# Kernel optimization log

Hardware: AMD Instinct MI355X
Metric: run time of the kernel (lower is better)

The kernel has to match this reference:

```python
import jax, jax.numpy as jnp
import numpy as np

N = 50000
IN_C = 128
HID = 64
HEADS = 4
OUT_C = 64
E_RAND = 800000
NEG_SLOPE = 0.2  # PyG GATConv default


def setup_inputs() -> dict:
    key = jax.random.key(0)
    ks = jax.random.split(key, 10)
    x = jax.random.normal(ks[0], (N, IN_C), dtype=jnp.float32)
    src = jax.random.randint(ks[1], (E_RAND,), 0, N)
    dst = jax.random.randint(ks[2], (E_RAND,), 0, N)
    loops = jnp.arange(N)
    # PyG GATConv adds self-loops by default; append them here
    edge_index = jnp.stack([jnp.concatenate([src, loops]),
                            jnp.concatenate([dst, loops])], axis=0).astype(jnp.int64)
    s = 0.05
    W1 = jax.random.normal(ks[3], (IN_C, HEADS * HID), dtype=jnp.float32) * s
    att_src1 = jax.random.normal(ks[4], (HEADS, HID), dtype=jnp.float32) * s
    att_dst1 = jax.random.normal(ks[5], (HEADS, HID), dtype=jnp.float32) * s
    b1 = jnp.zeros((HEADS * HID,), dtype=jnp.float32)
    W2 = jax.random.normal(ks[6], (HEADS * HID, OUT_C), dtype=jnp.float32) * s
    att_src2 = jax.random.normal(ks[7], (1, OUT_C), dtype=jnp.float32) * s
    att_dst2 = jax.random.normal(ks[8], (1, OUT_C), dtype=jnp.float32) * s
    b2 = jnp.zeros((OUT_C,), dtype=jnp.float32)
    return {"x": x, "edge_index": edge_index, "W1": W1, "att_src1": att_src1,
            "att_dst1": att_dst1, "b1": b1, "W2": W2, "att_src2": att_src2,
            "att_dst2": att_dst2, "b2": b2}


def gat_conv(x, src, dst, W, att_src, att_dst, bias, heads, ch, concat):
    n = x.shape[0]
    h = (x @ W).reshape(n, heads, ch)                      # [N,H,C]
    a_src = jnp.einsum('nhc,hc->nh', h, att_src)           # [N,H]
    a_dst = jnp.einsum('nhc,hc->nh', h, att_dst)
    e = jax.nn.leaky_relu(a_src[src] + a_dst[dst], NEG_SLOPE)  # [E,H]
    # segment softmax over incoming edges of each dst node
    m = jax.ops.segment_max(e, dst, num_segments=n)
    ex = jnp.exp(e - m[dst])
    ssum = jax.ops.segment_sum(ex, dst, num_segments=n)
    alpha = ex / jnp.where(ssum[dst] > 0, ssum[dst], 1.0)  # [E,H]
    msg = h[src] * alpha[:, :, None]                        # [E,H,C]
    out = jax.ops.segment_sum(msg, dst, num_segments=n)     # [N,H,C]
    out = out.reshape(n, heads * ch) if concat else out.mean(axis=1)
    return out + bias


def reference(x, edge_index, W1, att_src1, att_dst1, b1, W2, att_src2, att_dst2, b2):
    src, dst = edge_index[0], edge_index[1]
    # eval mode: feature dropout and attention dropout are identity
    h = gat_conv(x, src, dst, W1, att_src1, att_dst1, b1, HEADS, HID, True)
    h = jax.nn.elu(h)
    out = gat_conv(h, src, dst, W2, att_src2, att_dst2, b2, 1, OUT_C, False)
    return out
```

## Files before the change

kernel.cpp:

```cpp
#include <hip/hip_runtime.h>
#include <hip/hip_bf16.h>

#define IN_C 128
#define HID 64
#define HEADS 4
#define OUT_C 64
#define NEG_SLOPE 0.2f

typedef __attribute__((ext_vector_type(8))) short bfrag8;
typedef __attribute__((ext_vector_type(4))) float facc4;

__device__ __forceinline__ float bf16u_to_f(unsigned short u) {
  return __uint_as_float(((unsigned)u) << 16);
}
__device__ __forceinline__ unsigned short f_to_bf16u(float f) {
  return __bfloat16_as_ushort(__float2bfloat16(f));
}
__device__ __forceinline__ float leaky(float x) {
  return (x > 0.f) ? x : NEG_SLOPE * x;
}

__global__ __launch_bounds__(256) void cvt_w_kernel(
    const float* __restrict__ W1, const float* __restrict__ W2,
    unsigned short* __restrict__ B1img, unsigned short* __restrict__ B2img) {
  int i = blockIdx.x * 256 + threadIdx.x;
  if (i < 4096) {
    int g = i & 7, n = (i >> 3) & 255, kt = i >> 11;
    unsigned short q[8];
#pragma unroll
    for (int e = 0; e < 8; ++e)
      q[e] = f_to_bf16u(W1[(size_t)(kt * 64 + g * 8 + e) * 256 + n]);
    *reinterpret_cast<uint4*>(&B1img[kt * 16384 + n * 64 + ((g ^ (n & 7)) << 3)]) =
        *reinterpret_cast<const uint4*>(q);
  } else if (i < 4096 + 2048) {
    int j = i - 4096;
    int g = j & 7, n = (j >> 3) & 63, kt = j >> 9;
    unsigned short q[8];
#pragma unroll
    for (int e = 0; e < 8; ++e)
      q[e] = f_to_bf16u(W2[(size_t)(kt * 64 + g * 8 + e) * 64 + n]);
    *reinterpret_cast<uint4*>(&B2img[kt * 4096 + n * 64 + ((g ^ (n & 7)) << 3)]) =
        *reinterpret_cast<const uint4*>(q);
  }
}

__global__ __launch_bounds__(256) void mfma_gemm1_wide(
    const float* __restrict__ A, const unsigned short* __restrict__ B1img,
    const float* __restrict__ att_src, const float* __restrict__ att_dst,
    unsigned short* __restrict__ Hout, float* __restrict__ a_src,
    float* __restrict__ a_dst, int M) {
  __shared__ unsigned short As[64 * 64];
  __shared__ unsigned short Bs[256 * 64];
  const int t = threadIdx.x;
  const int wid = t >> 6, lane = t & 63;
  const int lg = lane >> 4, li = lane & 15;
  const int bm = blockIdx.x * 64;

  facc4 acc[16];
#pragma unroll
  for (int fn = 0; fn < 16; ++fn) acc[fn] = (facc4)(0.f);

#pragma unroll
  for (int kt = 0; kt < 2; ++kt) {
#pragma unroll
    for (int p = 0; p < 2; ++p) {
      int flat = t + p * 256;
      int row = flat >> 3, g = flat & 7;
      int gr = bm + row;
      float4 v0 = make_float4(0.f, 0.f, 0.f, 0.f), v1 = v0;
      if (gr < M) {
        const float* src = &A[(size_t)gr * 128 + kt * 64 + g * 8];
        v0 = *reinterpret_cast<const float4*>(src);
        v1 = *reinterpret_cast<const float4*>(src + 4);
      }
      unsigned short q[8];
      q[0] = f_to_bf16u(v0.x); q[1] = f_to_bf16u(v0.y);
      q[2] = f_to_bf16u(v0.z); q[3] = f_to_bf16u(v0.w);
      q[4] = f_to_bf16u(v1.x); q[5] = f_to_bf16u(v1.y);
      q[6] = f_to_bf16u(v1.z); q[7] = f_to_bf16u(v1.w);
      *reinterpret_cast<uint4*>(&As[row * 64 + ((g ^ (row & 7)) << 3)]) =
          *reinterpret_cast<const uint4*>(q);
    }
#pragma unroll
    for (int p = 0; p < 8; ++p) {
      int gi = t + p * 256;
      *reinterpret_cast<uint4*>(&Bs[gi * 8]) =
          *reinterpret_cast<const uint4*>(&B1img[kt * 16384 + gi * 8]);
    }
    __syncthreads();
#pragma unroll
    for (int ks = 0; ks < 2; ++ks) {
      int arow = wid * 16 + li;
      int gk = ks * 4 + lg;
      bfrag8 a = *reinterpret_cast<const bfrag8*>(
          &As[arow * 64 + ((gk ^ (arow & 7)) << 3)]);
#pragma unroll
      for (int fn = 0; fn < 16; ++fn) {
        int col = fn * 16 + li;
        bfrag8 b = *reinterpret_cast<const bfrag8*>(
            &Bs[col * 64 + ((gk ^ (col & 7)) << 3)]);
        acc[fn] =
            __builtin_amdgcn_mfma_f32_16x16x32_bf16(a, b, acc[fn], 0, 0, 0);
      }
    }
    __syncthreads();
  }

#pragma unroll
  for (int reg = 0; reg < 4; ++reg) {
    int row = bm + wid * 16 + lg * 4 + reg;
    if (row < M) {
#pragma unroll
      for (int fn = 0; fn < 16; ++fn)
        Hout[(size_t)row * 256 + fn * 16 + li] = f_to_bf16u(acc[fn][reg]);
    }
#pragma unroll
    for (int h = 0; h < 4; ++h) {
      float ps = 0.f, pd = 0.f;
#pragma unroll
      for (int q = 0; q < 4; ++q) {
        int fn = h * 4 + q;
        float c = acc[fn][reg];
        ps += c * att_src[fn * 16 + li];
        pd += c * att_dst[fn * 16 + li];
      }
#pragma unroll
      for (int m = 1; m < 16; m <<= 1) {
        ps += __shfl_xor(ps, m);
        pd += __shfl_xor(pd, m);
      }
      if (row < M && li == 0) {
        a_src[(size_t)row * 4 + h] = ps;
        a_dst[(size_t)row * 4 + h] = pd;
      }
    }
  }
}

__global__ __launch_bounds__(256) void mfma_gemm2(
    const unsigned short* __restrict__ A, const unsigned short* __restrict__ B2img,
    const float* __restrict__ att_src, const float* __restrict__ att_dst,
    unsigned short* __restrict__ Hout, float* __restrict__ a_src,
    float* __restrict__ a_dst, int M) {
  __shared__ unsigned short As[64 * 64];
  __shared__ unsigned short Bs[64 * 64];
  const int t = threadIdx.x;
  const int wid = t >> 6, lane = t & 63;
  const int lg = lane >> 4, li = lane & 15;
  const int bm = blockIdx.x * 64;

  facc4 acc[4];
#pragma unroll
  for (int fn = 0; fn < 4; ++fn) acc[fn] = (facc4)(0.f);

#pragma unroll
  for (int kt = 0; kt < 4; ++kt) {
#pragma unroll
    for (int p = 0; p < 2; ++p) {
      int flat = t + p * 256;
      int row = flat >> 3, g = flat & 7;
      int gr = bm + row;
      uint4 v = make_uint4(0, 0, 0, 0);
      if (gr < M)
        v = *reinterpret_cast<const uint4*>(&A[(size_t)gr * 256 + kt * 64 + g * 8]);
      *reinterpret_cast<uint4*>(&As[row * 64 + ((g ^ (row & 7)) << 3)]) = v;
    }
#pragma unroll
    for (int p = 0; p < 2; ++p) {
      int gi = t + p * 256;
      *reinterpret_cast<uint4*>(&Bs[gi * 8]) =
          *reinterpret_cast<const uint4*>(&B2img[kt * 4096 + gi * 8]);
    }
    __syncthreads();
#pragma unroll
    for (int ks = 0; ks < 2; ++ks) {
      int arow = wid * 16 + li;
      int gk = ks * 4 + lg;
      bfrag8 a = *reinterpret_cast<const bfrag8*>(
          &As[arow * 64 + ((gk ^ (arow & 7)) << 3)]);
#pragma unroll
      for (int fn = 0; fn < 4; ++fn) {
        int col = fn * 16 + li;
        bfrag8 b = *reinterpret_cast<const bfrag8*>(
            &Bs[col * 64 + ((gk ^ (col & 7)) << 3)]);
        acc[fn] =
            __builtin_amdgcn_mfma_f32_16x16x32_bf16(a, b, acc[fn], 0, 0, 0);
      }
    }
    __syncthreads();
  }

  float s_att[4], d_att[4];
#pragma unroll
  for (int fn = 0; fn < 4; ++fn) {
    s_att[fn] = att_src[fn * 16 + li];
    d_att[fn] = att_dst[fn * 16 + li];
  }
#pragma unroll
  for (int reg = 0; reg < 4; ++reg) {
    int row = bm + wid * 16 + lg * 4 + reg;
    float ps = 0.f, pd = 0.f;
#pragma unroll
    for (int fn = 0; fn < 4; ++fn) {
      float c = acc[fn][reg];
      ps += c * s_att[fn];
      pd += c * d_att[fn];
    }
#pragma unroll
    for (int m = 1; m < 16; m <<= 1) {
      ps += __shfl_xor(ps, m);
      pd += __shfl_xor(pd, m);
    }
    if (row < M) {
#pragma unroll
      for (int fn = 0; fn < 4; ++fn)
        Hout[(size_t)row * 64 + fn * 16 + li] = f_to_bf16u(acc[fn][reg]);
      if (li == 0) {
        a_src[row] = ps;
        a_dst[row] = pd;
      }
    }
  }
}

__global__ void hist_kernel(const int* __restrict__ dst, int E,
                            int* __restrict__ deg) {
  int e = blockIdx.x * blockDim.x + threadIdx.x;
  if (e < E) atomicAdd(&deg[dst[e]], 1);
}

__device__ __forceinline__ int pad4(int d) { return (d + 3) & ~3; }

__global__ __launch_bounds__(256) void scan_partial_kernel(
    const int* __restrict__ deg, int n, int* __restrict__ partials) {
  __shared__ int sm[256];
  int t = threadIdx.x;
  int i = blockIdx.x * 256 + t;
  sm[t] = (i < n) ? pad4(deg[i]) : 0;
  __syncthreads();
  for (int off = 128; off > 0; off >>= 1) {
    if (t < off) sm[t] += sm[t + off];
    __syncthreads();
  }
  if (t == 0) partials[blockIdx.x] = sm[0];
}

__global__ __launch_bounds__(256) void scan_expand_kernel(
    const int* __restrict__ deg, int n, const int* __restrict__ partials,
    int nb, int* __restrict__ offsets, int* __restrict__ cursor,
    int* __restrict__ ssrc) {
  __shared__ int smp[256];
  __shared__ int sm[256];
  int t = threadIdx.x;
  smp[t] = (t < nb) ? partials[t] : 0;
  __syncthreads();
  for (int off = 1; off < 256; off <<= 1) {
    int u = (t >= off) ? smp[t - off] : 0;
    __syncthreads();
    smp[t] += u;
    __syncthreads();
  }
  int base = (blockIdx.x > 0) ? smp[blockIdx.x - 1] : 0;
  int i = blockIdx.x * 256 + t;
  int d = (i < n) ? deg[i] : 0;
  int v = pad4(d);
  sm[t] = v;
  __syncthreads();
  for (int off = 1; off < 256; off <<= 1) {
    int u = (t >= off) ? sm[t - off] : 0;
    __syncthreads();
    sm[t] += u;
    __syncthreads();
  }
  int excl = sm[t] - v + base;
  if (i < n) {
    offsets[i] = excl;
    cursor[i] = excl;
    for (int k = d; k < v; ++k) ssrc[excl + k] = -1;
  }
}

__global__ void scatter_kernel(const int* __restrict__ src,
                               const int* __restrict__ dst, int E,
                               int* __restrict__ cursor,
                               int* __restrict__ ssrc) {
  int e = blockIdx.x * blockDim.x + threadIdx.x;
  if (e < E) {
    int d = dst[e];
    int pos = atomicAdd(&cursor[d], 1);
    ssrc[pos] = src[e];
  }
}

__global__ __launch_bounds__(256) void agg1_kernel(
    const unsigned short* __restrict__ h1, const float* __restrict__ as1,
    const float* __restrict__ ad1, const int* __restrict__ ssrc,
    const int* __restrict__ offsets, const int* __restrict__ deg,
    const float* __restrict__ bias, unsigned short* __restrict__ out,
    int n_nodes) {
  int wave = (int)((blockIdx.x * blockDim.x + threadIdx.x) >> 6);
  int lane = threadIdx.x & 63;
  if (wave >= n_nodes) return;
  int head = lane >> 4;
  int off = offsets[wave];
  int cnt = deg[wave];
  int last = ((cnt + 3) >> 2) - 1;
  const int* S_ = ssrc + off;
  float ad = ad1[wave * 4 + head];
  const int pbase = lane & 48;

  auto ldS = [&](int g) {
    return *reinterpret_cast<const int4*>(S_ + min(g, last) * 4);
  };
  auto gK = [&](int4 S, float* a_out) {
    int sk = (lane & 1) ? S.y : S.x;
    int sk2 = (lane & 1) ? S.w : S.z;
    sk = (lane & 2) ? sk2 : sk;
    *a_out = as1[max(sk, 0) * 4 + head];
    return sk;
  };
  auto mkP = [&](int sk, float a) {
    float pk = (sk >= 0) ? __expf(leaky(a + ad)) : 0.f;
    return make_float4(__shfl(pk, pbase), __shfl(pk, pbase + 1),
                       __shfl(pk, pbase + 2), __shfl(pk, pbase + 3));
  };
  auto gat = [&](int s) {
    return *reinterpret_cast<const ushort4*>(
        &h1[(size_t)max(s, 0) * 256 + lane * 4]);
  };

  int4 Sg0 = ldS(0), Sg1 = ldS(1), Sg2 = ldS(2), Sg3 = ldS(3);
  ushort4 H0 = gat(Sg0.x), H1 = gat(Sg0.y), H2 = gat(Sg0.z), H3 = gat(Sg0.w);
  ushort4 H4 = gat(Sg1.x), H5 = gat(Sg1.y), H6 = gat(Sg1.z), H7 = gat(Sg1.w);
  ushort4 H8 = gat(Sg2.x), H9 = gat(Sg2.y), H10 = gat(Sg2.z), H11 = gat(Sg2.w);
  float aK0, aK1, aK2;
  int sk0 = gK(Sg0, &aK0);
  int sk1 = gK(Sg1, &aK1);
  int sk2 = gK(Sg2, &aK2);
  float4 P0 = mkP(sk0, aK0), P1v = mkP(sk1, aK1);

  float l = 0.f, a0 = 0.f, a1 = 0.f, a2 = 0.f, a3 = 0.f;
  for (int j = 0; j <= last; ++j) {
    int4 Sg4 = ldS(j + 4);
    float aK3;
    int sk3 = gK(Sg3, &aK3);
    float4 P2v = mkP(sk2, aK2);
    l += P0.x + P0.y + P0.z + P0.w;
    a0 += P0.x * bf16u_to_f(H0.x) + P0.y * bf16u_to_f(H1.x) +
          P0.z * bf16u_to_f(H2.x) + P0.w * bf16u_to_f(H3.x);
    a1 += P0.x * bf16u_to_f(H0.y) + P0.y * bf16u_to_f(H1.y) +
          P0.z * bf16u_to_f(H2.y) + P0.w * bf16u_to_f(H3.y);
    a2 += P0.x * bf16u_to_f(H0.z) + P0.y * bf16u_to_f(H1.z) +
          P0.z * bf16u_to_f(H2.z) + P0.w * bf16u_to_f(H3.z);
    a3 += P0.x * bf16u_to_f(H0.w) + P0.y * bf16u_to_f(H1.w) +
          P0.z * bf16u_to_f(H2.w) + P0.w * bf16u_to_f(H3.w);
    H0 = H4; H1 = H5; H2 = H6; H3 = H7;
    H4 = H8; H5 = H9; H6 = H10; H7 = H11;
    H8 = gat(Sg3.x); H9 = gat(Sg3.y); H10 = gat(Sg3.z); H11 = gat(Sg3.w);
    Sg3 = Sg4;
    sk2 = sk3; aK2 = aK3;
    P0 = P1v; P1v = P2v;
  }
  float inv = 1.0f / l;
  int col = lane * 4;
  float4 b4 = *reinterpret_cast<const float4*>(&bias[col]);
  float o0 = a0 * inv + b4.x;
  float o1 = a1 * inv + b4.y;
  float o2 = a2 * inv + b4.z;
  float o3 = a3 * inv + b4.w;
  o0 = o0 > 0.f ? o0 : __expf(o0) - 1.f;
  o1 = o1 > 0.f ? o1 : __expf(o1) - 1.f;
  o2 = o2 > 0.f ? o2 : __expf(o2) - 1.f;
  o3 = o3 > 0.f ? o3 : __expf(o3) - 1.f;
  unsigned short q[4];
  q[0] = f_to_bf16u(o0); q[1] = f_to_bf16u(o1);
  q[2] = f_to_bf16u(o2); q[3] = f_to_bf16u(o3);
  *reinterpret_cast<ushort4*>(&out[(size_t)wave * 256 + col]) =
      *reinterpret_cast<const ushort4*>(q);
}

__global__ __launch_bounds__(256) void agg2_kernel(
    const unsigned short* __restrict__ h2, const float* __restrict__ as2,
    const float* __restrict__ ad2, const int* __restrict__ ssrc,
    const int* __restrict__ offsets, const int* __restrict__ deg,
    const float* __restrict__ bias, float* __restrict__ out, int n_nodes) {
  int wave = (int)((blockIdx.x * blockDim.x + threadIdx.x) >> 6);
  int lane = threadIdx.x & 63;
  if (wave >= n_nodes) return;
  int off = offsets[wave];
  int cnt = deg[wave];
  int last = ((cnt + 3) >> 2) - 1;
  const int* S_ = ssrc + off;
  float ad = ad2[wave];

  auto ldS = [&](int g) {
    return *reinterpret_cast<const int4*>(S_ + min(g, last) * 4);
  };
  auto gK = [&](int4 S, float* a_out) {
    int sk = (lane & 1) ? S.y : S.x;
    int sk2 = (lane & 1) ? S.w : S.z;
    sk = (lane & 2) ? sk2 : sk;
    *a_out = as2[max(sk, 0)];
    return sk;
  };
  auto mkP = [&](int sk, float a) {
    float pk = (sk >= 0) ? __expf(leaky(a + ad)) : 0.f;
    return make_float4(__shfl(pk, 0), __shfl(pk, 1), __shfl(pk, 2),
                       __shfl(pk, 3));
  };
  auto gat = [&](int s) { return h2[(size_t)max(s, 0) * 64 + lane]; };

  int4 Sg0 = ldS(0), Sg1 = ldS(1), Sg2 = ldS(2), Sg3 = ldS(3);
  unsigned short H0 = gat(Sg0.x), H1 = gat(Sg0.y), H2 = gat(Sg0.z),
                 H3 = gat(Sg0.w);
  unsigned short H4 = gat(Sg1.x), H5 = gat(Sg1.y), H6 = gat(Sg1.z),
                 H7 = gat(Sg1.w);
  unsigned short H8 = gat(Sg2.x), H9 = gat(Sg2.y), H10 = gat(Sg2.z),
                 H11 = gat(Sg2.w);
  float aK0, aK1, aK2;
  int sk0 = gK(Sg0, &aK0);
  int sk1 = gK(Sg1, &aK1);
  int sk2 = gK(Sg2, &aK2);
  float4 P0 = mkP(sk0, aK0), P1v = mkP(sk1, aK1);

  float l = 0.f, acc = 0.f;
  for (int j = 0; j <= last; ++j) {
    int4 Sg4 = ldS(j + 4);
    float aK3;
    int sk3 = gK(Sg3, &aK3);
    float4 P2v = mkP(sk2, aK2);
    l += P0.x + P0.y + P0.z + P0.w;
    acc += P0.x * bf16u_to_f(H0) + P0.y * bf16u_to_f(H1) +
           P0.z * bf16u_to_f(H2) + P0.w * bf16u_to_f(H3);
    H0 = H4; H1 = H5; H2 = H6; H3 = H7;
    H4 = H8; H5 = H9; H6 = H10; H7 = H11;
    H8 = gat(Sg3.x); H9 = gat(Sg3.y); H10 = gat(Sg3.z); H11 = gat(Sg3.w);
    Sg3 = Sg4;
    sk2 = sk3; aK2 = aK3;
    P0 = P1v; P1v = P2v;
  }
  out[(size_t)wave * 64 + lane] = acc / l + bias[lane];
}

extern "C" void kernel_launch(void* const* d_in, const int* in_sizes, int n_in,
                              void* d_out, int out_size, void* d_ws,
                              size_t ws_size, hipStream_t stream) {
  const float* x = (const float*)d_in[0];
  const int* edge_index = (const int*)d_in[1];
  const float* W1 = (const float*)d_in[2];
  const float* att_src1 = (const float*)d_in[3];
  const float* att_dst1 = (const float*)d_in[4];
  const float* b1 = (const float*)d_in[5];
  const float* W2 = (const float*)d_in[6];
  const float* att_src2 = (const float*)d_in[7];
  const float* att_dst2 = (const float*)d_in[8];
  const float* b2 = (const float*)d_in[9];

  const int n = in_sizes[0] / IN_C;
  const int E = in_sizes[1] / 2;
  const int* src = edge_index;
  const int* dst = edge_index + E;
  const int nb = (n + 255) / 256;
  const int stride = (E + 4 * n + 3) & ~3;

  char* ws = (char*)d_ws;
  size_t off = 0;
  auto carve = [&](size_t bytes) -> void* {
    void* p = ws + off;
    off = (off + bytes + 255) & ~(size_t)255;
    return p;
  };
  unsigned short* h1b = (unsigned short*)carve((size_t)n * 256 * 2);
  unsigned short* hact = (unsigned short*)carve((size_t)n * 256 * 2);
  unsigned short* h2b = (unsigned short*)carve((size_t)n * 64 * 2);
  unsigned short* B1img = (unsigned short*)carve(32768 * 2);
  unsigned short* B2img = (unsigned short*)carve(16384 * 2);
  float* as1 = (float*)carve((size_t)n * 4 * 4);
  float* ad1 = (float*)carve((size_t)n * 4 * 4);
  float* as2 = (float*)carve((size_t)n * 4);
  float* ad2 = (float*)carve((size_t)n * 4);
  int* deg = (int*)carve((size_t)n * 4);
  int* offsets = (int*)carve((size_t)n * 4);
  int* cursor = (int*)carve((size_t)n * 4);
  int* ssrc = (int*)carve((size_t)stride * 4);
  int* partials = (int*)carve((size_t)nb * 4);

  hipMemsetAsync(deg, 0, (size_t)n * 4, stream);

  cvt_w_kernel<<<24, 256, 0, stream>>>(W1, W2, B1img, B2img);
  mfma_gemm1_wide<<<(n + 63) / 64, 256, 0, stream>>>(
      x, B1img, att_src1, att_dst1, h1b, as1, ad1, n);
  hist_kernel<<<(E + 255) / 256, 256, 0, stream>>>(dst, E, deg);
  scan_partial_kernel<<<nb, 256, 0, stream>>>(deg, n, partials);
  scan_expand_kernel<<<nb, 256, 0, stream>>>(deg, n, partials, nb, offsets,
                                             cursor, ssrc);
  scatter_kernel<<<(E + 255) / 256, 256, 0, stream>>>(src, dst, E, cursor,
                                                      ssrc);
  agg1_kernel<<<(n * 64 + 255) / 256, 256, 0, stream>>>(
      h1b, as1, ad1, ssrc, offsets, deg, b1, hact, n);
  mfma_gemm2<<<(n + 63) / 64, 256, 0, stream>>>(hact, B2img, att_src2,
                                                att_dst2, h2b, as2, ad2, n);
  agg2_kernel<<<(n * 64 + 255) / 256, 256, 0, stream>>>(
      h2b, as2, ad2, ssrc, offsets, deg, b2, (float*)d_out, n);
}
```

Baseline: 312.8 us.

## Record atomic rank in histogram, drop scatter atomics, double-buffer aggregation gathers

```diff
diff --git a/kernel.cpp b/kernel.cpp
--- a/kernel.cpp
+++ b/kernel.cpp
@@ -12,6 +12,12 @@
 
 __device__ __forceinline__ float bf16u_to_f(unsigned short u) {
   return __uint_as_float(((unsigned)u) << 16);
+}
+__device__ __forceinline__ float lof(unsigned u) {
+  return __uint_as_float(u << 16);
+}
+__device__ __forceinline__ float hif(unsigned u) {
+  return __uint_as_float(u & 0xffff0000u);
 }
 __device__ __forceinline__ unsigned short f_to_bf16u(float f) {
   return __bfloat16_as_ushort(__float2bfloat16(f));
@@ -223,10 +229,10 @@
   }
 }
 
-__global__ void hist_kernel(const int* __restrict__ dst, int E,
-                            int* __restrict__ deg) {
+__global__ void hist_rank_kernel(const int* __restrict__ dst, int E,
+                                 int* __restrict__ deg, int* __restrict__ rank) {
   int e = blockIdx.x * blockDim.x + threadIdx.x;
-  if (e < E) atomicAdd(&deg[dst[e]], 1);
+  if (e < E) rank[e] = atomicAdd(&deg[dst[e]], 1);
 }
 
 __device__ __forceinline__ int pad4(int d) { return (d + 3) & ~3; }
@@ -247,8 +253,7 @@
 
 __global__ __launch_bounds__(256) void scan_expand_kernel(
     const int* __restrict__ deg, int n, const int* __restrict__ partials,
-    int nb, int* __restrict__ offsets, int* __restrict__ cursor,
-    int* __restrict__ ssrc) {
+    int nb, int* __restrict__ offsets, int* __restrict__ ssrc) {
   __shared__ int smp[256];
   __shared__ int sm[256];
   int t = threadIdx.x;
@@ -275,21 +280,17 @@
   int excl = sm[t] - v + base;
   if (i < n) {
     offsets[i] = excl;
-    cursor[i] = excl;
     for (int k = d; k < v; ++k) ssrc[excl + k] = -1;
   }
 }
 
 __global__ void scatter_kernel(const int* __restrict__ src,
-                               const int* __restrict__ dst, int E,
-                               int* __restrict__ cursor,
+                               const int* __restrict__ dst,
+                               const int* __restrict__ rank,
+                               const int* __restrict__ offsets, int E,
                                int* __restrict__ ssrc) {
   int e = blockIdx.x * blockDim.x + threadIdx.x;
-  if (e < E) {
-    int d = dst[e];
-    int pos = atomicAdd(&cursor[d], 1);
-    ssrc[pos] = src[e];
-  }
+  if (e < E) ssrc[offsets[dst[e]] + rank[e]] = src[e];
 }
 
 __global__ __launch_bounds__(256) void agg1_kernel(
@@ -325,42 +326,46 @@
                        __shfl(pk, pbase + 2), __shfl(pk, pbase + 3));
   };
   auto gat = [&](int s) {
-    return *reinterpret_cast<const ushort4*>(
+    return *reinterpret_cast<const uint2*>(
         &h1[(size_t)max(s, 0) * 256 + lane * 4]);
   };
 
-  int4 Sg0 = ldS(0), Sg1 = ldS(1), Sg2 = ldS(2), Sg3 = ldS(3);
-  ushort4 H0 = gat(Sg0.x), H1 = gat(Sg0.y), H2 = gat(Sg0.z), H3 = gat(Sg0.w);
-  ushort4 H4 = gat(Sg1.x), H5 = gat(Sg1.y), H6 = gat(Sg1.z), H7 = gat(Sg1.w);
-  ushort4 H8 = gat(Sg2.x), H9 = gat(Sg2.y), H10 = gat(Sg2.z), H11 = gat(Sg2.w);
-  float aK0, aK1, aK2;
-  int sk0 = gK(Sg0, &aK0);
-  int sk1 = gK(Sg1, &aK1);
-  int sk2 = gK(Sg2, &aK2);
-  float4 P0 = mkP(sk0, aK0), P1v = mkP(sk1, aK1);
-
   float l = 0.f, a0 = 0.f, a1 = 0.f, a2 = 0.f, a3 = 0.f;
-  for (int j = 0; j <= last; ++j) {
-    int4 Sg4 = ldS(j + 4);
-    float aK3;
-    int sk3 = gK(Sg3, &aK3);
-    float4 P2v = mkP(sk2, aK2);
-    l += P0.x + P0.y + P0.z + P0.w;
-    a0 += P0.x * bf16u_to_f(H0.x) + P0.y * bf16u_to_f(H1.x) +
-          P0.z * bf16u_to_f(H2.x) + P0.w * bf16u_to_f(H3.x);
-    a1 += P0.x * bf16u_to_f(H0.y) + P0.y * bf16u_to_f(H1.y) +
-          P0.z * bf16u_to_f(H2.y) + P0.w * bf16u_to_f(H3.y);
-    a2 += P0.x * bf16u_to_f(H0.z) + P0.y * bf16u_to_f(H1.z) +
-          P0.z * bf16u_to_f(H2.z) + P0.w * bf16u_to_f(H3.z);
-    a3 += P0.x * bf16u_to_f(H0.w) + P0.y * bf16u_to_f(H1.w) +
-          P0.z * bf16u_to_f(H2.w) + P0.w * bf16u_to_f(H3.w);
-    H0 = H4; H1 = H5; H2 = H6; H3 = H7;
-    H4 = H8; H5 = H9; H6 = H10; H7 = H11;
-    H8 = gat(Sg3.x); H9 = gat(Sg3.y); H10 = gat(Sg3.z); H11 = gat(Sg3.w);
-    Sg3 = Sg4;
-    sk2 = sk3; aK2 = aK3;
-    P0 = P1v; P1v = P2v;
-  }
+
+  int4 Sg0 = ldS(0), Sg1 = ldS(1);
+  int4 SgP = ldS(2);
+  uint2 HA0 = gat(Sg0.x), HA1 = gat(Sg0.y), HA2 = gat(Sg0.z), HA3 = gat(Sg0.w);
+  uint2 HB0 = gat(Sg1.x), HB1 = gat(Sg1.y), HB2 = gat(Sg1.z), HB3 = gat(Sg1.w);
+  float aKA, aKB;
+  int skA = gK(Sg0, &aKA);
+  int skB = gK(Sg1, &aKB);
+  float4 PA = mkP(skA, aKA), PB;
+
+  int j = 0;
+  auto step = [&](float4& Pc, float4& Pn, uint2& Hc0, uint2& Hc1, uint2& Hc2,
+                  uint2& Hc3, int& skN, float& aKN, int skC, float aKC) {
+    Pn = mkP(skC, aKC);
+    skN = gK(SgP, &aKN);
+    l += Pc.x + Pc.y + Pc.z + Pc.w;
+    a0 += Pc.x * lof(Hc0.x) + Pc.y * lof(Hc1.x) + Pc.z * lof(Hc2.x) +
+          Pc.w * lof(Hc3.x);
+    a1 += Pc.x * hif(Hc0.x) + Pc.y * hif(Hc1.x) + Pc.z * hif(Hc2.x) +
+          Pc.w * hif(Hc3.x);
+    a2 += Pc.x * lof(Hc0.y) + Pc.y * lof(Hc1.y) + Pc.z * lof(Hc2.y) +
+          Pc.w * lof(Hc3.y);
+    a3 += Pc.x * hif(Hc0.y) + Pc.y * hif(Hc1.y) + Pc.z * hif(Hc2.y) +
+          Pc.w * hif(Hc3.y);
+    Hc0 = gat(SgP.x); Hc1 = gat(SgP.y); Hc2 = gat(SgP.z); Hc3 = gat(SgP.w);
+    SgP = ldS(j + 3);
+  };
+
+  for (;;) {
+    step(PA, PB, HA0, HA1, HA2, HA3, skA, aKA, skB, aKB);
+    if (++j > last) break;
+    step(PB, PA, HB0, HB1, HB2, HB3, skB, aKB, skA, aKA);
+    if (++j > last) break;
+  }
+
   float inv = 1.0f / l;
   int col = lane * 4;
   float4 b4 = *reinterpret_cast<const float4*>(&bias[col]);
@@ -410,35 +415,39 @@
   };
   auto gat = [&](int s) { return h2[(size_t)max(s, 0) * 64 + lane]; };
 
-  int4 Sg0 = ldS(0), Sg1 = ldS(1), Sg2 = ldS(2), Sg3 = ldS(3);
-  unsigned short H0 = gat(Sg0.x), H1 = gat(Sg0.y), H2 = gat(Sg0.z),
-                 H3 = gat(Sg0.w);
-  unsigned short H4 = gat(Sg1.x), H5 = gat(Sg1.y), H6 = gat(Sg1.z),
-                 H7 = gat(Sg1.w);
-  unsigned short H8 = gat(Sg2.x), H9 = gat(Sg2.y), H10 = gat(Sg2.z),
-                 H11 = gat(Sg2.w);
-  float aK0, aK1, aK2;
-  int sk0 = gK(Sg0, &aK0);
-  int sk1 = gK(Sg1, &aK1);
-  int sk2 = gK(Sg2, &aK2);
-  float4 P0 = mkP(sk0, aK0), P1v = mkP(sk1, aK1);
-
   float l = 0.f, acc = 0.f;
-  for (int j = 0; j <= last; ++j) {
-    int4 Sg4 = ldS(j + 4);
-    float aK3;
-    int sk3 = gK(Sg3, &aK3);
-    float4 P2v = mkP(sk2, aK2);
-    l += P0.x + P0.y + P0.z + P0.w;
-    acc += P0.x * bf16u_to_f(H0) + P0.y * bf16u_to_f(H1) +
-           P0.z * bf16u_to_f(H2) + P0.w * bf16u_to_f(H3);
-    H0 = H4; H1 = H5; H2 = H6; H3 = H7;
-    H4 = H8; H5 = H9; H6 = H10; H7 = H11;
-    H8 = gat(Sg3.x); H9 = gat(Sg3.y); H10 = gat(Sg3.z); H11 = gat(Sg3.w);
-    Sg3 = Sg4;
-    sk2 = sk3; aK2 = aK3;
-    P0 = P1v; P1v = P2v;
-  }
+
+  int4 Sg0 = ldS(0), Sg1 = ldS(1);
+  int4 SgP = ldS(2);
+  unsigned short HA0 = gat(Sg0.x), HA1 = gat(Sg0.y), HA2 = gat(Sg0.z),
+                 HA3 = gat(Sg0.w);
+  unsigned short HB0 = gat(Sg1.x), HB1 = gat(Sg1.y), HB2 = gat(Sg1.z),
+                 HB3 = gat(Sg1.w);
+  float aKA, aKB;
+  int skA = gK(Sg0, &aKA);
+  int skB = gK(Sg1, &aKB);
+  float4 PA = mkP(skA, aKA), PB;
+
+  int j = 0;
+  auto step = [&](float4& Pc, float4& Pn, unsigned short& Hc0,
+                  unsigned short& Hc1, unsigned short& Hc2, unsigned short& Hc3,
+                  int& skN, float& aKN, int skC, float aKC) {
+    Pn = mkP(skC, aKC);
+    skN = gK(SgP, &aKN);
+    l += Pc.x + Pc.y + Pc.z + Pc.w;
+    acc += Pc.x * bf16u_to_f(Hc0) + Pc.y * bf16u_to_f(Hc1) +
+           Pc.z * bf16u_to_f(Hc2) + Pc.w * bf16u_to_f(Hc3);
+    Hc0 = gat(SgP.x); Hc1 = gat(SgP.y); Hc2 = gat(SgP.z); Hc3 = gat(SgP.w);
+    SgP = ldS(j + 3);
+  };
+
+  for (;;) {
+    step(PA, PB, HA0, HA1, HA2, HA3, skA, aKA, skB, aKB);
+    if (++j > last) break;
+    step(PB, PA, HB0, HB1, HB2, HB3, skB, aKB, skA, aKA);
+    if (++j > last) break;
+  }
+
   out[(size_t)wave * 64 + lane] = acc / l + bias[lane];
 }
 
@@ -481,7 +490,7 @@
   float* ad2 = (float*)carve((size_t)n * 4);
   int* deg = (int*)carve((size_t)n * 4);
   int* offsets = (int*)carve((size_t)n * 4);
-  int* cursor = (int*)carve((size_t)n * 4);
+  int* rank = (int*)carve((size_t)E * 4);
   int* ssrc = (int*)carve((size_t)stride * 4);
   int* partials = (int*)carve((size_t)nb * 4);
 
@@ -490,12 +499,12 @@
   cvt_w_kernel<<<24, 256, 0, stream>>>(W1, W2, B1img, B2img);
   mfma_gemm1_wide<<<(n + 63) / 64, 256, 0, stream>>>(
       x, B1img, att_src1, att_dst1, h1b, as1, ad1, n);
-  hist_kernel<<<(E + 255) / 256, 256, 0, stream>>>(dst, E, deg);
+  hist_rank_kernel<<<(E + 255) / 256, 256, 0, stream>>>(dst, E, deg, rank);
   scan_partial_kernel<<<nb, 256, 0, stream>>>(deg, n, partials);
   scan_expand_kernel<<<nb, 256, 0, stream>>>(deg, n, partials, nb, offsets,
-                                             cursor, ssrc);
-  scatter_kernel<<<(E + 255) / 256, 256, 0, stream>>>(src, dst, E, cursor,
-                                                      ssrc);
+                                             ssrc);
+  scatter_kernel<<<(E + 255) / 256, 256, 0, stream>>>(src, dst, rank, offsets,
+                                                      E, ssrc);
   agg1_kernel<<<(n * 64 + 255) / 256, 256, 0, stream>>>(
       h1b, as1, ad1, ssrc, offsets, deg, b1, hact, n);
   mfma_gemm2<<<(n + 63) / 64, 256, 0, stream>>>(hact, B2img, att_src2,
```

Measured after the change: 273.3 us. -12.6%, faster.
